# Kernel optimization log

Measured on AMD Instinct MI355X. Metric: run time of the kernel, lower is better.

Reference implementation:

```python
import jax, jax.numpy as jnp
import numpy as np

# Hyperparameters from __init__
NOISE = 0.1
DT = 10.0
TAU_MIN = 10.0
TAU_MAX = 100.0
TAU_RANGE = TAU_MAX - TAU_MIN
B, T, I, H = 64, 512, 256, 1024


def setup_inputs() -> dict:
    key = jax.random.key(0)
    k0, k1, k2, k3, k4 = jax.random.split(key, 5)
    x = jax.random.normal(k0, (B, T, I), dtype=jnp.float32)
    # pre-sampled standard-normal noise (replaces torch.randn_like per step)
    noise_eps = jax.random.normal(k1, (B, T, H), dtype=jnp.float32)
    # in_fc: Linear(input_size, hidden_size)
    in_w = jax.random.normal(k2, (H, I), dtype=jnp.float32) * np.float32(1.0 / np.sqrt(I))
    in_b = jnp.zeros((H,), dtype=jnp.float32)
    # W: xavier_normal_ init -> std = sqrt(2/(fan_in+fan_out))
    W = jax.random.normal(k3, (H, H), dtype=jnp.float32) * np.float32(np.sqrt(2.0 / (H + H)))
    # taus param initialized as sigmoid(rand)*range+min; stored raw then re-sigmoided in recurrence.
    taus = jax.nn.sigmoid(jax.random.uniform(k4, (H,), dtype=jnp.float32)) * TAU_RANGE + TAU_MIN
    return {"x": x, "noise_eps": noise_eps, "in_w": in_w, "in_b": in_b, "W": W, "taus": taus}


def reference(x, noise_eps, in_w, in_b, W, taus):
    # alpha is time-invariant: compute once outside the scan
    tau = jax.nn.sigmoid(taus) * TAU_RANGE + TAU_MIN      # [H]
    alpha = DT / tau                                      # [H]
    # input projection has no sequential dependency: batch it over time
    inp_proj = jnp.einsum('bti,hi->bth', x, in_w) + in_b  # [B,T,H]
    h0 = jnp.zeros((x.shape[0], W.shape[0]), dtype=x.dtype)

    def step(h, inputs):
        pt, eps = inputs                                  # [B,H] each
        h = (1.0 - alpha) * h + alpha * jnp.tanh(pt + h @ W + eps * NOISE)
        return h, h

    xs = (jnp.swapaxes(inp_proj, 0, 1), jnp.swapaxes(noise_eps, 0, 1))  # time-major
    _, hs = jax.lax.scan(step, h0, xs)                    # hs: [T,B,H]
    return jnp.swapaxes(hs, 0, 1)                         # [B,T,H]
```

## Files before the change

### kernel.cpp

```cpp
#include <hip/hip_runtime.h>

typedef short short8 __attribute__((ext_vector_type(8)));
typedef float floatx4 __attribute__((ext_vector_type(4)));
typedef unsigned short u16;
typedef unsigned u32;
typedef unsigned long long u64;

#define MFMA16 __builtin_amdgcn_mfma_f32_16x16x32_bf16

#define B_  64
#define T_  512
#define I_  256
#define H_  1024
#define CNT_STRIDE 64
#define XS_STRIDE 272
#define HS_STRIDE 1040

__device__ __forceinline__ u16 rne_bf(float f) {
    union { float f; u32 i; } v; v.f = f;
    return (u16)((v.i + 0x7fffu + ((v.i >> 16) & 1u)) >> 16);
}
__device__ __forceinline__ void split_bf(float f, u16& hi, u16& lo) {
    u16 h = rne_bf(f);
    union { u32 i; float f; } hf; hf.i = ((u32)h) << 16;
    hi = h;
    lo = rne_bf(f - hf.f);
}
__device__ __forceinline__ void split4(float4 v, u64& hi64, u64& lo64) {
    u16 h0,l0,h1,l1,h2,l2,h3,l3;
    split_bf(v.x,h0,l0); split_bf(v.y,h1,l1);
    split_bf(v.z,h2,l2); split_bf(v.w,h3,l3);
    hi64 = (u64)h0 | ((u64)h1 << 16) | ((u64)h2 << 32) | ((u64)h3 << 48);
    lo64 = (u64)l0 | ((u64)l1 << 16) | ((u64)l2 << 32) | ((u64)l3 << 48);
}

__global__ __launch_bounds__(256, 1) void leaky_rnn(
    const float* __restrict__ x, const float* __restrict__ eps,
    const float* __restrict__ in_w, const float* __restrict__ in_b,
    const float* __restrict__ W, const float* __restrict__ taus,
    float* __restrict__ out, float* __restrict__ hbf, unsigned* __restrict__ cnt)
{
    __shared__ float Wl[128 * 68];
    __shared__ u16 xs_hi[4 * XS_STRIDE];
    __shared__ u16 xs_lo[4 * XS_STRIDE];
    __shared__ u16 hs_hi[4 * HS_STRIDE];
    __shared__ u16 hs_lo[4 * HS_STRIDE];

    const int tid  = threadIdx.x;
    const int wave = tid >> 6;
    const int lane = tid & 63;
    const int n    = lane & 15;
    const int quad = lane >> 4;
    const int g    = blockIdx.x & 15;
    const int cb   = blockIdx.x >> 4;
    const int jme  = cb * 64 + wave * 16 + n;

    short8 whi[32], wlo[32];
    #pragma unroll
    for (int ph = 0; ph < 8; ++ph) {
        #pragma unroll
        for (int ii = 0; ii < 8; ++ii) {
            int f4i = ii * 256 + tid;
            int row = f4i >> 4, c4 = (f4i & 15) * 4;
            *(float4*)(Wl + row * 68 + c4) =
                *(const float4*)(W + (size_t)(ph * 128 + row) * H_ + cb * 64 + c4);
        }
        __syncthreads();
        #pragma unroll
        for (int ckl = 0; ckl < 4; ++ckl) {
            short8 fh, fl;
            #pragma unroll
            for (int i = 0; i < 8; ++i) {
                float v = Wl[(ckl * 32 + quad * 8 + i) * 68 + wave * 16 + n];
                u16 h, l; split_bf(v, h, l);
                fh[i] = (short)h; fl[i] = (short)l;
            }
            whi[ph * 4 + ckl] = fh;
            wlo[ph * 4 + ckl] = fl;
        }
        __syncthreads();
    }

    short8 iwhi[8], iwlo[8];
    #pragma unroll
    for (int ck = 0; ck < 8; ++ck) {
        float4 a = *(const float4*)(in_w + (size_t)jme * I_ + ck * 32 + quad * 8);
        float4 b = *(const float4*)(in_w + (size_t)jme * I_ + ck * 32 + quad * 8 + 4);
        short8 fh, fl;
        float vv[8] = {a.x, a.y, a.z, a.w, b.x, b.y, b.z, b.w};
        #pragma unroll
        for (int i = 0; i < 8; ++i) {
            u16 h, l; split_bf(vv[i], h, l);
            fh[i] = (short)h; fl[i] = (short)l;
        }
        iwhi[ck] = fh; iwlo[ck] = fl;
    }

    float tv = taus[jme];
    float sg = 1.0f / (1.0f + __expf(-tv));
    float al = 10.0f / (sg * 90.0f + 10.0f);
    float om = 1.0f - al;
    float bj = in_b[jme];
    float hm[4] = {0.f, 0.f, 0.f, 0.f};

    unsigned* myc = cnt + g * CNT_STRIDE;

    #pragma unroll 1
    for (int t = 0; t < T_; ++t) {
        float epr[4];
        if (quad == 0) {
            #pragma unroll
            for (int r = 0; r < 4; ++r)
                epr[r] = eps[((g * 4 + r) * T_ + t) * H_ + jme];
        }
        {
            int b = tid >> 6, c = (tid & 63) * 4;
            float4 xv = *(const float4*)(x + ((g * 4 + b) * T_ + t) * I_ + c);
            u64 hi64, lo64; split4(xv, hi64, lo64);
            *(u64*)(xs_hi + b * XS_STRIDE + c) = hi64;
            *(u64*)(xs_lo + b * XS_STRIDE + c) = lo64;
        }
        __syncthreads();

        if (tid == 0 && t > 0) {
            unsigned tgt = 16u * (unsigned)t;
            while (__hip_atomic_load(myc, __ATOMIC_RELAXED, __HIP_MEMORY_SCOPE_AGENT) < tgt)
                __builtin_amdgcn_s_sleep(1);
        }
        __syncthreads();

        u64 hv[8];
        {
            u64* src8 = (u64*)(hbf + (size_t)((t & 1) * 16 + g) * 4096);
            #pragma unroll
            for (int ii = 0; ii < 8; ++ii)
                hv[ii] = __hip_atomic_load(src8 + ii * 256 + tid,
                                           __ATOMIC_RELAXED, __HIP_MEMORY_SCOPE_AGENT);
        }

        floatx4 acc[8];
        #pragma unroll
        for (int a8 = 0; a8 < 8; ++a8) { floatx4 z = {0.f,0.f,0.f,0.f}; acc[a8] = z; }
        {
            const u16* xh = xs_hi + (n & 3) * XS_STRIDE + quad * 8;
            const u16* xl = xs_lo + (n & 3) * XS_STRIDE + quad * 8;
            #pragma unroll
            for (int ck = 0; ck < 8; ++ck) {
                short8 ah  = *(const short8*)(xh + ck * 32);
                short8 al8 = *(const short8*)(xl + ck * 32);
                acc[ck] = MFMA16(ah, iwhi[ck], acc[ck], 0, 0, 0);
                acc[ck] = MFMA16(ah, iwlo[ck], acc[ck], 0, 0, 0);
                acc[ck] = MFMA16(al8, iwhi[ck], acc[ck], 0, 0, 0);
            }
        }

        {
            #pragma unroll
            for (int ii = 0; ii < 8; ++ii) {
                int idx = ii * 256 + tid;
                int b = idx >> 9, c = (idx & 511) * 2;
                float f0 = __uint_as_float((u32)hv[ii]);
                float f1 = __uint_as_float((u32)(hv[ii] >> 32));
                u16 h0, l0, h1, l1;
                split_bf(f0, h0, l0); split_bf(f1, h1, l1);
                *(u32*)(hs_hi + b * HS_STRIDE + c) = (u32)h0 | ((u32)h1 << 16);
                *(u32*)(hs_lo + b * HS_STRIDE + c) = (u32)l0 | ((u32)l1 << 16);
            }
        }
        __syncthreads();

        {
            const u16* hh = hs_hi + (n & 3) * HS_STRIDE + quad * 8;
            const u16* hl = hs_lo + (n & 3) * HS_STRIDE + quad * 8;
            #pragma unroll
            for (int ck = 0; ck < 32; ++ck) {
                short8 ah  = *(const short8*)(hh + ck * 32);
                short8 al8 = *(const short8*)(hl + ck * 32);
                acc[ck & 7] = MFMA16(ah, whi[ck], acc[ck & 7], 0, 0, 0);
                acc[ck & 7] = MFMA16(ah, wlo[ck], acc[ck & 7], 0, 0, 0);
                acc[ck & 7] = MFMA16(al8, whi[ck], acc[ck & 7], 0, 0, 0);
            }
        }

        if (quad == 0) {
            float* dst = hbf + (size_t)(((t + 1) & 1) * 16 + g) * 4096;
            #pragma unroll
            for (int r = 0; r < 4; ++r) {
                float pre = acc[0][r] + acc[1][r] + acc[2][r] + acc[3][r]
                          + acc[4][r] + acc[5][r] + acc[6][r] + acc[7][r]
                          + bj + 0.1f * epr[r];
                float ex = __expf(2.0f * pre);
                float th = 1.0f - 2.0f / (ex + 1.0f);
                hm[r] = om * hm[r] + al * th;
                out[((g * 4 + r) * T_ + t) * H_ + jme] = hm[r];
                __hip_atomic_store((u32*)(dst + r * H_ + jme), __float_as_uint(hm[r]),
                                   __ATOMIC_RELAXED, __HIP_MEMORY_SCOPE_AGENT);
            }
        }
        __syncthreads();
        if (tid == 0)
            __hip_atomic_fetch_add(myc, 1u, __ATOMIC_RELAXED, __HIP_MEMORY_SCOPE_AGENT);
    }
}

extern "C" void kernel_launch(void* const* d_in, const int* in_sizes, int n_in,
                              void* d_out, int out_size, void* d_ws, size_t ws_size,
                              hipStream_t stream) {
    const float* x    = (const float*)d_in[0];
    const float* eps  = (const float*)d_in[1];
    const float* in_w = (const float*)d_in[2];
    const float* in_b = (const float*)d_in[3];
    const float* W    = (const float*)d_in[4];
    const float* taus = (const float*)d_in[5];
    float* out = (float*)d_out;

    unsigned* cnt = (unsigned*)d_ws;
    float* hbf = (float*)((char*)d_ws + 4096);

    hipMemsetAsync(d_ws, 0, 4096 + 16 * 4096 * sizeof(float), stream);

    leaky_rnn<<<dim3(256), dim3(256), 0, stream>>>(x, eps, in_w, in_b, W, taus,
                                                   out, hbf, cnt);
}
```

Baseline: 2.526 ms.

## Replace counter barrier with per-element step-tagged hidden state flags

Drops the global atomic counter and its spin-wait plus two block barriers per step. Each hidden element is now published as a 64-bit word that holds the pre-split bf16 hi/lo pair and a timestep tag, and readers poll until every element carries the current step. The next step's x and noise loads are prefetched during the recurrent matmul. MFMA accumulator assignment is interleaved to shorten dependency chains. The cost is double the exchange traffic per element and more register pressure from holding 16 values in flight, plus a buffer-size change in the memset.

```diff
diff --git a/kernel.cpp b/kernel.cpp
--- a/kernel.cpp
+++ b/kernel.cpp
@@ -12,7 +12,6 @@
 #define T_  512
 #define I_  256
 #define H_  1024
-#define CNT_STRIDE 64
 #define XS_STRIDE 272
 #define HS_STRIDE 1040
 
@@ -38,7 +37,7 @@
     const float* __restrict__ x, const float* __restrict__ eps,
     const float* __restrict__ in_w, const float* __restrict__ in_b,
     const float* __restrict__ W, const float* __restrict__ taus,
-    float* __restrict__ out, float* __restrict__ hbf, unsigned* __restrict__ cnt)
+    float* __restrict__ out, u64* __restrict__ hbf, unsigned* __restrict__ cnt)
 {
     __shared__ float Wl[128 * 68];
     __shared__ u16 xs_hi[4 * XS_STRIDE];
@@ -103,40 +102,34 @@
     float bj = in_b[jme];
     float hm[4] = {0.f, 0.f, 0.f, 0.f};
 
-    unsigned* myc = cnt + g * CNT_STRIDE;
+    float4 xv;
+    float epr[4] = {0.f, 0.f, 0.f, 0.f};
+    {
+        int b = tid >> 6, c = (tid & 63) * 4;
+        xv = *(const float4*)(x + ((size_t)(g * 4 + b) * T_ + 0) * I_ + c);
+    }
+    if (quad == 0) {
+        #pragma unroll
+        for (int r = 0; r < 4; ++r)
+            epr[r] = eps[((size_t)(g * 4 + r) * T_ + 0) * H_ + jme];
+    }
 
     #pragma unroll 1
     for (int t = 0; t < T_; ++t) {
-        float epr[4];
-        if (quad == 0) {
-            #pragma unroll
-            for (int r = 0; r < 4; ++r)
-                epr[r] = eps[((g * 4 + r) * T_ + t) * H_ + jme];
-        }
         {
             int b = tid >> 6, c = (tid & 63) * 4;
-            float4 xv = *(const float4*)(x + ((g * 4 + b) * T_ + t) * I_ + c);
             u64 hi64, lo64; split4(xv, hi64, lo64);
             *(u64*)(xs_hi + b * XS_STRIDE + c) = hi64;
             *(u64*)(xs_lo + b * XS_STRIDE + c) = lo64;
         }
         __syncthreads();
 
-        if (tid == 0 && t > 0) {
-            unsigned tgt = 16u * (unsigned)t;
-            while (__hip_atomic_load(myc, __ATOMIC_RELAXED, __HIP_MEMORY_SCOPE_AGENT) < tgt)
-                __builtin_amdgcn_s_sleep(1);
-        }
-        __syncthreads();
-
-        u64 hv[8];
-        {
-            u64* src8 = (u64*)(hbf + (size_t)((t & 1) * 16 + g) * 4096);
-            #pragma unroll
-            for (int ii = 0; ii < 8; ++ii)
-                hv[ii] = __hip_atomic_load(src8 + ii * 256 + tid,
-                                           __ATOMIC_RELAXED, __HIP_MEMORY_SCOPE_AGENT);
-        }
+        u64 hv[16];
+        u64* src8 = hbf + ((size_t)(t & 1) * 16 + g) * 4096;
+        #pragma unroll
+        for (int ii = 0; ii < 16; ++ii)
+            hv[ii] = __hip_atomic_load(src8 + ii * 256 + tid,
+                                       __ATOMIC_RELAXED, __HIP_MEMORY_SCOPE_AGENT);
 
         floatx4 acc[8];
         #pragma unroll
@@ -148,26 +141,50 @@
             for (int ck = 0; ck < 8; ++ck) {
                 short8 ah  = *(const short8*)(xh + ck * 32);
                 short8 al8 = *(const short8*)(xl + ck * 32);
-                acc[ck] = MFMA16(ah, iwhi[ck], acc[ck], 0, 0, 0);
-                acc[ck] = MFMA16(ah, iwlo[ck], acc[ck], 0, 0, 0);
-                acc[ck] = MFMA16(al8, iwhi[ck], acc[ck], 0, 0, 0);
-            }
-        }
-
-        {
-            #pragma unroll
-            for (int ii = 0; ii < 8; ++ii) {
-                int idx = ii * 256 + tid;
-                int b = idx >> 9, c = (idx & 511) * 2;
-                float f0 = __uint_as_float((u32)hv[ii]);
-                float f1 = __uint_as_float((u32)(hv[ii] >> 32));
-                u16 h0, l0, h1, l1;
-                split_bf(f0, h0, l0); split_bf(f1, h1, l1);
-                *(u32*)(hs_hi + b * HS_STRIDE + c) = (u32)h0 | ((u32)h1 << 16);
-                *(u32*)(hs_lo + b * HS_STRIDE + c) = (u32)l0 | ((u32)l1 << 16);
-            }
-        }
-        __syncthreads();
+                acc[(3*ck+0)&7] = MFMA16(ah,  iwhi[ck], acc[(3*ck+0)&7], 0, 0, 0);
+                acc[(3*ck+1)&7] = MFMA16(ah,  iwlo[ck], acc[(3*ck+1)&7], 0, 0, 0);
+                acc[(3*ck+2)&7] = MFMA16(al8, iwhi[ck], acc[(3*ck+2)&7], 0, 0, 0);
+            }
+        }
+
+        {
+            u32 pend = 0;
+            #pragma unroll
+            for (int ii = 0; ii < 16; ++ii)
+                if ((u32)(hv[ii] >> 48) != (u32)t) pend |= (1u << ii);
+            while (pend) {
+                #pragma unroll
+                for (int ii = 0; ii < 16; ++ii)
+                    if (pend & (1u << ii))
+                        hv[ii] = __hip_atomic_load(src8 + ii * 256 + tid,
+                                                   __ATOMIC_RELAXED, __HIP_MEMORY_SCOPE_AGENT);
+                #pragma unroll
+                for (int ii = 0; ii < 16; ++ii)
+                    if ((u32)(hv[ii] >> 48) == (u32)t) pend &= ~(1u << ii);
+            }
+        }
+
+        #pragma unroll
+        for (int ii = 0; ii < 16; ++ii) {
+            int idx = ii * 256 + tid;
+            int b = idx >> 10, c = idx & 1023;
+            hs_hi[b * HS_STRIDE + c] = (u16)hv[ii];
+            hs_lo[b * HS_STRIDE + c] = (u16)(hv[ii] >> 16);
+        }
+        __syncthreads();
+
+        float4 xvn;
+        float eprn[4] = {0.f, 0.f, 0.f, 0.f};
+        {
+            int tn = (t < T_ - 1) ? t + 1 : t;
+            int b = tid >> 6, c = (tid & 63) * 4;
+            xvn = *(const float4*)(x + ((size_t)(g * 4 + b) * T_ + tn) * I_ + c);
+            if (quad == 0) {
+                #pragma unroll
+                for (int r = 0; r < 4; ++r)
+                    eprn[r] = eps[((size_t)(g * 4 + r) * T_ + tn) * H_ + jme];
+            }
+        }
 
         {
             const u16* hh = hs_hi + (n & 3) * HS_STRIDE + quad * 8;
@@ -176,14 +193,14 @@
             for (int ck = 0; ck < 32; ++ck) {
                 short8 ah  = *(const short8*)(hh + ck * 32);
                 short8 al8 = *(const short8*)(hl + ck * 32);
-                acc[ck & 7] = MFMA16(ah, whi[ck], acc[ck & 7], 0, 0, 0);
-                acc[ck & 7] = MFMA16(ah, wlo[ck], acc[ck & 7], 0, 0, 0);
-                acc[ck & 7] = MFMA16(al8, whi[ck], acc[ck & 7], 0, 0, 0);
+                acc[(3*ck+0)&7] = MFMA16(ah,  whi[ck], acc[(3*ck+0)&7], 0, 0, 0);
+                acc[(3*ck+1)&7] = MFMA16(ah,  wlo[ck], acc[(3*ck+1)&7], 0, 0, 0);
+                acc[(3*ck+2)&7] = MFMA16(al8, whi[ck], acc[(3*ck+2)&7], 0, 0, 0);
             }
         }
 
         if (quad == 0) {
-            float* dst = hbf + (size_t)(((t + 1) & 1) * 16 + g) * 4096;
+            u64* dst8 = hbf + ((size_t)((t + 1) & 1) * 16 + g) * 4096;
             #pragma unroll
             for (int r = 0; r < 4; ++r) {
                 float pre = acc[0][r] + acc[1][r] + acc[2][r] + acc[3][r]
@@ -192,14 +209,17 @@
                 float ex = __expf(2.0f * pre);
                 float th = 1.0f - 2.0f / (ex + 1.0f);
                 hm[r] = om * hm[r] + al * th;
-                out[((g * 4 + r) * T_ + t) * H_ + jme] = hm[r];
-                __hip_atomic_store((u32*)(dst + r * H_ + jme), __float_as_uint(hm[r]),
+                out[((size_t)(g * 4 + r) * T_ + t) * H_ + jme] = hm[r];
+                u16 ph, pl; split_bf(hm[r], ph, pl);
+                u64 pk = (u64)ph | ((u64)pl << 16) | ((u64)(u32)(t + 1) << 48);
+                __hip_atomic_store(dst8 + r * 1024 + jme, pk,
                                    __ATOMIC_RELAXED, __HIP_MEMORY_SCOPE_AGENT);
             }
         }
-        __syncthreads();
-        if (tid == 0)
-            __hip_atomic_fetch_add(myc, 1u, __ATOMIC_RELAXED, __HIP_MEMORY_SCOPE_AGENT);
+
+        xv = xvn;
+        #pragma unroll
+        for (int r = 0; r < 4; ++r) epr[r] = eprn[r];
     }
 }
 
@@ -215,9 +235,9 @@
     float* out = (float*)d_out;
 
     unsigned* cnt = (unsigned*)d_ws;
-    float* hbf = (float*)((char*)d_ws + 4096);
-
-    hipMemsetAsync(d_ws, 0, 4096 + 16 * 4096 * sizeof(float), stream);
+    u64* hbf = (u64*)((char*)d_ws + 4096);
+
+    hipMemsetAsync(d_ws, 0, 4096 + 2 * 16 * 4096 * sizeof(u64), stream);
 
     leaky_rnn<<<dim3(256), dim3(256), 0, stream>>>(x, eps, in_w, in_b, W, taus,
                                                    out, hbf, cnt);
```

Result: faster. 2.358 ms (-6.7%).
